# Performance work log

Hardware: AMD Instinct MI355X
Metric: run time of the kernel (lower is better)

## Reference

```python
import jax, jax.numpy as jnp
import numpy as np
from jax import lax

D = 1024      # input_dim
H = 4096      # hidden_dim (4*D)
E = 8         # num_experts
TOPK = 2      # sparse_top_k


def setup_inputs() -> dict:
    key = jax.random.key(0)
    ks = jax.random.split(key, 7)
    s = 0.02
    return {
        "x": jax.random.normal(ks[0], (2, 2048, D), dtype=jnp.float32),
        "W1": jax.random.normal(ks[1], (E, D, H), dtype=jnp.float32) * s,
        "b1": jnp.zeros((E, H), dtype=jnp.float32),
        "W2": jax.random.normal(ks[2], (E, H, D), dtype=jnp.float32) * s,
        "b2": jnp.zeros((E, D), dtype=jnp.float32),
        "Wr": jax.random.normal(ks[3], (D, E), dtype=jnp.float32) * s,
        "br": jnp.zeros((E,), dtype=jnp.float32),
    }


def reference(x, W1, b1, W2, b2, Wr, br):
    B, S, _ = x.shape
    xf = x.reshape(-1, D)                                  # [T, D]
    logits = xf @ Wr + br                                  # [T, E]
    # top-k threshold masking (keep logits >= k-th largest, else -inf)
    topv, _ = lax.top_k(logits, TOPK)                      # [T, k]
    thresh = topv[:, TOPK - 1:TOPK]                        # [T, 1]
    masked = jnp.where(logits >= thresh, logits, -jnp.inf)
    weights = jax.nn.softmax(masked, axis=-1)              # [T, E]
    # run ALL experts densely (faithful to reference), then weighted sum
    h = jax.nn.gelu(jnp.einsum('td,edh->eth', xf, W1) + b1[:, None, :],
                    approximate=False)                     # [E, T, H]
    expert_out = jnp.einsum('eth,ehd->etd', h, W2) + b2[:, None, :]  # [E, T, D]
    out = jnp.einsum('etd,te->td', expert_out, weights)    # [T, D]
    return out.reshape(B, S, D)
```

## Files before the change

kernel.cpp:

```cpp
#include <hip/hip_runtime.h>
#include <math.h>

typedef __bf16 bf16x8 __attribute__((ext_vector_type(8)));
typedef float f32x4 __attribute__((ext_vector_type(4)));

#define DDIM 1024
#define HDIM 4096
#define NE 8
#define TT 4096
#define CAP 9216

static const size_t OFF_CTRL   = 0;
static const size_t OFF_ROWMAP = 256;
static const size_t OFF_WROW   = OFF_ROWMAP + (size_t)CAP * 4;
static const size_t OFF_ROWPOS = OFF_WROW + (size_t)CAP * 4;
static const size_t OFF_TOKE   = OFF_ROWPOS + (size_t)TT * 2 * 4;
static const size_t OFF_TOKW   = OFF_TOKE + (size_t)TT * 2 * 4;
static const size_t OFF_XB     = OFF_TOKW + (size_t)TT * 2 * 4;
static const size_t OFF_W1T    = OFF_XB + (size_t)TT * DDIM * 2;
static const size_t OFF_W2T    = OFF_W1T + (size_t)NE * HDIM * DDIM * 2;
static const size_t OFF_H      = OFF_W2T + (size_t)NE * DDIM * HDIM * 2;
static const size_t OFF_PO     = OFF_H + (size_t)CAP * HDIM * 2;
static const size_t WS_NEED    = OFF_PO + (size_t)CAP * DDIM * 2;

__device__ __forceinline__ unsigned short f2bf(float f) {
  unsigned int u = __builtin_bit_cast(unsigned int, f);
  u = (u + 0x7FFFu + ((u >> 16) & 1u)) >> 16;
  return (unsigned short)u;
}

__device__ __forceinline__ float bf2f(unsigned short s) {
  return __builtin_bit_cast(float, (unsigned int)s << 16);
}

__device__ __forceinline__ void async16(void* lds, const void* g) {
  __builtin_amdgcn_global_load_lds(
      (__attribute__((address_space(1))) void*)g,
      (__attribute__((address_space(3))) void*)lds, 16, 0, 0);
}

__device__ __forceinline__ float gelu_exact(float v) {
  return 0.5f * v * (1.0f + erff(v * 0.70710678118654752f));
}

__global__ __launch_bounds__(256) void router_k(
    const float* __restrict__ x, const float* __restrict__ Wr, const float* __restrict__ br,
    unsigned short* __restrict__ xb, int* __restrict__ toke, float* __restrict__ tokw) {
  int tid = threadIdx.x, lane = tid & 63, wid = tid >> 6;
  int t = blockIdx.x * 4 + wid;
  const float* xr = x + (size_t)t * DDIM;
  float acc[NE];
#pragma unroll
  for (int e = 0; e < NE; ++e) acc[e] = 0.f;
#pragma unroll
  for (int it = 0; it < DDIM / 256; ++it) {
    int d0 = it * 256 + lane * 4;
    float4 xv = *(const float4*)(xr + d0);
    ushort4 xs;
    xs.x = f2bf(xv.x); xs.y = f2bf(xv.y); xs.z = f2bf(xv.z); xs.w = f2bf(xv.w);
    *(ushort4*)(xb + (size_t)t * DDIM + d0) = xs;
    const float4* w0 = (const float4*)(Wr + (size_t)(d0 + 0) * NE);
    const float4* w1 = (const float4*)(Wr + (size_t)(d0 + 1) * NE);
    const float4* w2 = (const float4*)(Wr + (size_t)(d0 + 2) * NE);
    const float4* w3 = (const float4*)(Wr + (size_t)(d0 + 3) * NE);
    float4 a, b;
    a = w0[0]; b = w0[1];
    acc[0] += xv.x * a.x; acc[1] += xv.x * a.y; acc[2] += xv.x * a.z; acc[3] += xv.x * a.w;
    acc[4] += xv.x * b.x; acc[5] += xv.x * b.y; acc[6] += xv.x * b.z; acc[7] += xv.x * b.w;
    a = w1[0]; b = w1[1];
    acc[0] += xv.y * a.x; acc[1] += xv.y * a.y; acc[2] += xv.y * a.z; acc[3] += xv.y * a.w;
    acc[4] += xv.y * b.x; acc[5] += xv.y * b.y; acc[6] += xv.y * b.z; acc[7] += xv.y * b.w;
    a = w2[0]; b = w2[1];
    acc[0] += xv.z * a.x; acc[1] += xv.z * a.y; acc[2] += xv.z * a.z; acc[3] += xv.z * a.w;
    acc[4] += xv.z * b.x; acc[5] += xv.z * b.y; acc[6] += xv.z * b.z; acc[7] += xv.z * b.w;
    a = w3[0]; b = w3[1];
    acc[0] += xv.w * a.x; acc[1] += xv.w * a.y; acc[2] += xv.w * a.z; acc[3] += xv.w * a.w;
    acc[4] += xv.w * b.x; acc[5] += xv.w * b.y; acc[6] += xv.w * b.z; acc[7] += xv.w * b.w;
  }
#pragma unroll
  for (int e = 0; e < NE; ++e) {
#pragma unroll
    for (int s = 32; s > 0; s >>= 1) acc[e] += __shfl_xor(acc[e], s, 64);
  }
  if (lane == 0) {
    float l[NE];
#pragma unroll
    for (int e = 0; e < NE; ++e) l[e] = acc[e] + br[e];
    int i0 = 0; float m0 = l[0];
#pragma unroll
    for (int e = 1; e < NE; ++e) if (l[e] > m0) { m0 = l[e]; i0 = e; }
    int i1 = -1; float m1 = -3.4e38f;
#pragma unroll
    for (int e = 0; e < NE; ++e) if (e != i0 && l[e] > m1) { m1 = l[e]; i1 = e; }
    float e1 = expf(m1 - m0);
    float s = 1.f + e1;
    toke[2 * t] = i0;  toke[2 * t + 1] = i1;
    tokw[2 * t] = 1.f / s;  tokw[2 * t + 1] = e1 / s;
  }
}

__global__ __launch_bounds__(1024) void bin_k(
    const int* __restrict__ toke, const float* __restrict__ tokw,
    int* __restrict__ ctrl, int* __restrict__ rowmap,
    float* __restrict__ wrow, int* __restrict__ rowpos) {
  __shared__ int wcnt[16][8];
  __shared__ int wpre[16][8];
  __shared__ int pbase[9];
  __shared__ int ecnt[8];
  __shared__ int ebase[8];
  int tid = threadIdx.x, lane = tid & 63, w = tid >> 6;

  int myCnt = 0;
  for (int c = 0; c < 8; ++c) {
    int e = toke[c * 1024 + tid];
#pragma unroll
    for (int ee = 0; ee < 8; ++ee) {
      unsigned long long m = __ballot(e == ee);
      if (lane == ee) myCnt += (int)__popcll(m);
    }
  }
  if (lane < 8) wcnt[w][lane] = myCnt;
  __syncthreads();
  if (tid == 0) {
    int off = 0;
    for (int e = 0; e < 8; ++e) {
      int s = 0;
      for (int ww = 0; ww < 16; ++ww) s += wcnt[ww][e];
      ecnt[e] = s;
      pbase[e] = off;
      ebase[e] = off;
      ctrl[8 + e] = off;
      off += ((s + 127) >> 7) << 7;
    }
    pbase[8] = off;
    ctrl[16] = off;
  }
  __syncthreads();

  for (int e = 0; e < 8; ++e) {
    int start = pbase[e] + ecnt[e], end = pbase[e + 1];
    for (int r = start + tid; r < end; r += 1024) { rowmap[r] = 0; wrow[r] = 0.f; }
  }

  for (int c = 0; c < 8; ++c) {
    int slot = c * 1024 + tid;
    int e = toke[slot];
    unsigned long long mown = 0;
#pragma unroll
    for (int ee = 0; ee < 8; ++ee) {
      unsigned long long m = __ballot(e == ee);
      if (lane == ee) wcnt[w][ee] = (int)__popcll(m);
      if (e == ee) mown = m;
    }
    __syncthreads();
    if (tid < 128) {
      int ww = tid >> 3, ee = tid & 7;
      int s = 0;
      for (int p = 0; p < ww; ++p) s += wcnt[p][ee];
      wpre[ww][ee] = s;
    }
    __syncthreads();
    int rank = (int)__popcll(mown & ((1ull << lane) - 1ull));
    int r = ebase[e] + wpre[w][e] + rank;
    rowmap[r] = slot >> 1;
    wrow[r] = tokw[slot];
    rowpos[slot] = r;
    __syncthreads();
    if (tid < 8) {
      int s = 0;
      for (int ww = 0; ww < 16; ++ww) s += wcnt[ww][tid];
      ebase[tid] += s;
    }
    __syncthreads();
  }
}

__global__ __launch_bounds__(256) void convT_k(
    const float* __restrict__ src, unsigned short* __restrict__ dst, int K_, int N_) {
  __shared__ unsigned int lds32[64][33];
  int e = blockIdx.z;
  int kb = blockIdx.y << 6, nb = blockIdx.x << 6;
  int t = threadIdx.x;
  const float* s = src + (size_t)e * K_ * N_ + (size_t)kb * N_ + nb;
  int n0 = (t & 15) << 2;
#pragma unroll
  for (int i = 0; i < 2; ++i) {
    int k2 = (i << 4) + (t >> 4);
    float4 a = *(const float4*)(s + (size_t)(2 * k2) * N_ + n0);
    float4 b = *(const float4*)(s + (size_t)(2 * k2 + 1) * N_ + n0);
    lds32[n0 + 0][k2] = (unsigned)f2bf(a.x) | ((unsigned)f2bf(b.x) << 16);
    lds32[n0 + 1][k2] = (unsigned)f2bf(a.y) | ((unsigned)f2bf(b.y) << 16);
    lds32[n0 + 2][k2] = (unsigned)f2bf(a.z) | ((unsigned)f2bf(b.z) << 16);
    lds32[n0 + 3][k2] = (unsigned)f2bf(a.w) | ((unsigned)f2bf(b.w) << 16);
  }
  __syncthreads();
  unsigned short* dp = dst + (size_t)e * (size_t)N_ * K_ + (size_t)nb * K_ + kb;
  int n = t >> 2, c = t & 3;
  uint4 v0, v1;
  v0.x = lds32[n][(c << 2) + 0]; v0.y = lds32[n][(c << 2) + 1];
  v0.z = lds32[n][(c << 2) + 2]; v0.w = lds32[n][(c << 2) + 3];
  int c4 = (c + 4) << 2;
  v1.x = lds32[n][c4 + 0]; v1.y = lds32[n][c4 + 1];
  v1.z = lds32[n][c4 + 2]; v1.w = lds32[n][c4 + 3];
  *(uint4*)(dp + (size_t)n * K_ + (c << 3)) = v0;
  *(uint4*)(dp + (size_t)n * K_ + ((c + 4) << 3)) = v1;
}

template <int KTOT, int NTOT, bool GATHER, bool DOGELU, bool KSPLIT2>
__global__ __launch_bounds__(256, 2) void gemm_k(
    const unsigned short* __restrict__ A, const unsigned short* __restrict__ Bt,
    const int* __restrict__ ctrl, const int* __restrict__ rowmap,
    const float* __restrict__ wrow, const float* __restrict__ bias,
    unsigned short* __restrict__ out0, unsigned short* __restrict__ out1) {
  __shared__ __align__(16) char SMEM[32768];
  unsigned short* Asm = (unsigned short*)SMEM;
  unsigned short* Bsm = (unsigned short*)(SMEM + 16384);
  int zz = blockIdx.z;
  int e = KSPLIT2 ? (zz & 7) : zz;
  int ks = KSPLIT2 ? (zz >> 3) : 0;
  int off0 = ctrl[8 + e], off1 = ctrl[8 + e + 1];
  int row0 = off0 + (blockIdx.y << 7);
  if (row0 >= off1) return;
  int col0 = blockIdx.x << 7;
  int tid = threadIdx.x, lane = tid & 63, wid = tid >> 6;
  int wr = wid >> 1, wc = wid & 1;
  int kbeg = KSPLIT2 ? ks * (KTOT / 2) : 0;
  int kend = KSPLIT2 ? kbeg + (KTOT / 2) : KTOT;
  unsigned short* outp = (KSPLIT2 && ks) ? out1 : out0;
  if (DOGELU) outp = out0;

  const unsigned short* Asrc[4];
  const unsigned short* Bsrc[4];
#pragma unroll
  for (int c = 0; c < 4; ++c) {
    int ar = row0 + (c << 5) + (tid >> 3);
    size_t arow = GATHER ? (size_t)rowmap[ar] : (size_t)ar;
    Asrc[c] = A + arow * KTOT + ((tid & 7) << 3);
    int brw = col0 + (c << 5) + (tid >> 3);
    Bsrc[c] = Bt + ((size_t)e * NTOT + brw) * KTOT + ((tid & 7) << 3);
  }

  f32x4 acc[4][4];
#pragma unroll
  for (int m = 0; m < 4; ++m)
#pragma unroll
    for (int n = 0; n < 4; ++n) acc[m][n] = (f32x4){0.f, 0.f, 0.f, 0.f};

  int arow_rd = ((wr << 6) + (lane & 15)) << 6;
  int brow_rd = ((wc << 6) + (lane & 15)) << 6;
  int koff = (lane >> 4) << 3;

  for (int k0 = kbeg; k0 < kend; k0 += 64) {
#pragma unroll
    for (int c = 0; c < 4; ++c) {
      async16(SMEM + (((c << 8) + (wid << 6)) << 4), Asrc[c] + k0);
      async16(SMEM + 16384 + (((c << 8) + (wid << 6)) << 4), Bsrc[c] + k0);
    }
    __syncthreads();
#pragma unroll
    for (int kk = 0; kk < 64; kk += 32) {
      bf16x8 af[4], bfr[4];
#pragma unroll
      for (int m = 0; m < 4; ++m)
        af[m] = *(const bf16x8*)&Asm[arow_rd + (m << 10) + kk + koff];
#pragma unroll
      for (int n = 0; n < 4; ++n)
        bfr[n] = *(const bf16x8*)&Bsm[brow_rd + (n << 10) + kk + koff];
#pragma unroll
      for (int m = 0; m < 4; ++m)
#pragma unroll
        for (int n = 0; n < 4; ++n)
          acc[m][n] = __builtin_amdgcn_mfma_f32_16x16x32_bf16(af[m], bfr[n], acc[m][n], 0, 0, 0);
    }
    __syncthreads();
  }

  unsigned short (*Cl)[128] = (unsigned short(*)[128])SMEM;
  int r_b = (lane >> 4) << 2;
  int c_b = lane & 15;
#pragma unroll
  for (int n = 0; n < 4; ++n) {
    int col_l = (wc << 6) + (n << 4) + c_b;
    float bv = (KSPLIT2 && ks) ? 0.f : bias[e * NTOT + col0 + col_l];
#pragma unroll
    for (int m = 0; m < 4; ++m) {
#pragma unroll
      for (int r = 0; r < 4; ++r) {
        int row_l = (wr << 6) + (m << 4) + r_b + r;
        float v = acc[m][n][r] + bv;
        if (DOGELU) {
          Cl[row_l][col_l] = f2bf(gelu_exact(v));
        } else {
          Cl[row_l][col_l] = f2bf(wrow[row0 + row_l] * v);
        }
      }
    }
  }
  __syncthreads();
  int rb = tid >> 4, cof = (tid & 15) << 3;
#pragma unroll
  for (int j = 0; j < 8; ++j) {
    int row_l = rb + (j << 4);
    uint4 v = *(const uint4*)&Cl[row_l][cof];
    *(uint4*)&outp[(size_t)(row0 + row_l) * NTOT + col0 + cof] = v;
  }
}

__global__ __launch_bounds__(256) void gather_k(
    const unsigned short* __restrict__ p0, const unsigned short* __restrict__ p1,
    const int* __restrict__ rowpos, float* __restrict__ out) {
  int t = blockIdx.x, d = threadIdx.x << 2;
  int r0 = rowpos[2 * t], r1 = rowpos[2 * t + 1];
  ushort4 a0 = *(const ushort4*)&p0[(size_t)r0 * DDIM + d];
  ushort4 a1 = *(const ushort4*)&p1[(size_t)r0 * DDIM + d];
  ushort4 b0 = *(const ushort4*)&p0[(size_t)r1 * DDIM + d];
  ushort4 b1 = *(const ushort4*)&p1[(size_t)r1 * DDIM + d];
  float4 o;
  o.x = (bf2f(a0.x) + bf2f(a1.x)) + (bf2f(b0.x) + bf2f(b1.x));
  o.y = (bf2f(a0.y) + bf2f(a1.y)) + (bf2f(b0.y) + bf2f(b1.y));
  o.z = (bf2f(a0.z) + bf2f(a1.z)) + (bf2f(b0.z) + bf2f(b1.z));
  o.w = (bf2f(a0.w) + bf2f(a1.w)) + (bf2f(b0.w) + bf2f(b1.w));
  *(float4*)&out[(size_t)t * DDIM + d] = o;
}

extern "C" void kernel_launch(void* const* d_in, const int* in_sizes, int n_in,
                              void* d_out, int out_size, void* d_ws, size_t ws_size,
                              hipStream_t stream) {
  const float* x  = (const float*)d_in[0];
  const float* W1 = (const float*)d_in[1];
  const float* b1 = (const float*)d_in[2];
  const float* W2 = (const float*)d_in[3];
  const float* b2 = (const float*)d_in[4];
  const float* Wr = (const float*)d_in[5];
  const float* br = (const float*)d_in[6];
  float* out = (float*)d_out;

  if (ws_size < WS_NEED) return;

  char* ws = (char*)d_ws;
  int* ctrl            = (int*)(ws + OFF_CTRL);
  int* rowmap          = (int*)(ws + OFF_ROWMAP);
  float* wrow          = (float*)(ws + OFF_WROW);
  int* rowpos          = (int*)(ws + OFF_ROWPOS);
  int* toke            = (int*)(ws + OFF_TOKE);
  float* tokw          = (float*)(ws + OFF_TOKW);
  unsigned short* xb   = (unsigned short*)(ws + OFF_XB);
  unsigned short* W1T  = (unsigned short*)(ws + OFF_W1T);
  unsigned short* W2T  = (unsigned short*)(ws + OFF_W2T);
  unsigned short* hbuf = (unsigned short*)(ws + OFF_H);
  unsigned short* pout = (unsigned short*)(ws + OFF_PO);
  unsigned short* pout2 = (unsigned short*)(ws + OFF_W1T);

  router_k<<<TT / 4, 256, 0, stream>>>(x, Wr, br, xb, toke, tokw);
  bin_k<<<1, 1024, 0, stream>>>(toke, tokw, ctrl, rowmap, wrow, rowpos);

  convT_k<<<dim3(HDIM / 64, DDIM / 64, NE), 256, 0, stream>>>(W1, W1T, DDIM, HDIM);
  convT_k<<<dim3(DDIM / 64, HDIM / 64, NE), 256, 0, stream>>>(W2, W2T, HDIM, DDIM);

  gemm_k<DDIM, HDIM, true, true, false><<<dim3(HDIM / 128, 32, NE), 256, 0, stream>>>(
      xb, W1T, ctrl, rowmap, wrow, b1, hbuf, nullptr);
  gemm_k<HDIM, DDIM, false, false, true><<<dim3(DDIM / 128, 32, NE * 2), 256, 0, stream>>>(
      hbuf, W2T, ctrl, rowmap, wrow, b2, pout, pout2);

  gather_k<<<TT, 256, 0, stream>>>(pout, pout2, rowpos, out);
}
```

Baseline: 374.6 us.

## Replace first expert GEMM with 256x256-tile, 8-wave, double-buffered pipelined kernel

```diff
diff --git a/kernel.cpp b/kernel.cpp
--- a/kernel.cpp
+++ b/kernel.cpp
@@ -206,36 +206,164 @@
   *(uint4*)(dp + (size_t)n * K_ + ((c + 4) << 3)) = v1;
 }
 
-template <int KTOT, int NTOT, bool GATHER, bool DOGELU, bool KSPLIT2>
-__global__ __launch_bounds__(256, 2) void gemm_k(
+__global__ __launch_bounds__(512, 2) void gemm1_8p(
     const unsigned short* __restrict__ A, const unsigned short* __restrict__ Bt,
     const int* __restrict__ ctrl, const int* __restrict__ rowmap,
-    const float* __restrict__ wrow, const float* __restrict__ bias,
+    const float* __restrict__ bias, unsigned short* __restrict__ outb) {
+  __shared__ __align__(16) char SMEM[131072];
+  int e = blockIdx.z;
+  int off0 = ctrl[8 + e], off1 = ctrl[8 + e + 1];
+  int row0 = off0 + (blockIdx.y << 8);
+  if (row0 >= off1) return;
+  int col0 = blockIdx.x << 8;
+  int tid = threadIdx.x, lane = tid & 63, wid = tid >> 6;
+  int wm = wid >> 2, wn = wid & 3;
+
+  int r_lo = tid >> 2;
+  int ch = (tid & 3) ^ ((r_lo >> 1) & 3);
+  int ar0 = row0 + r_lo;       if (ar0 > off1 - 1) ar0 = off1 - 1;
+  int ar1 = row0 + r_lo + 128; if (ar1 > off1 - 1) ar1 = off1 - 1;
+  const unsigned short* As0 = A + (size_t)rowmap[ar0] * DDIM + (ch << 3);
+  const unsigned short* As1 = A + (size_t)rowmap[ar1] * DDIM + (ch << 3);
+  const unsigned short* Bs0 = Bt + ((size_t)e * HDIM + col0 + r_lo) * DDIM + (ch << 3);
+  const unsigned short* Bs1 = Bt + ((size_t)e * HDIM + col0 + r_lo + 128) * DDIM + (ch << 3);
+  int dstB = tid << 4;
+
+  int rl = lane & 15;
+  int chr = (((lane >> 4) ^ ((rl >> 1) & 3)) << 4);
+  int offA[8], offB[4];
+#pragma unroll
+  for (int m = 0; m < 8; ++m) offA[m] = ((wm << 7) + (m << 4) + rl) * 64 + chr;
+#pragma unroll
+  for (int n = 0; n < 4; ++n) offB[n] = ((wn << 6) + (n << 4) + rl) * 64 + chr;
+
+  f32x4 acc[8][4];
+#pragma unroll
+  for (int m = 0; m < 8; ++m)
+#pragma unroll
+    for (int n = 0; n < 4; ++n) acc[m][n] = (f32x4){0.f, 0.f, 0.f, 0.f};
+  bf16x8 afr[4], bfr[4];
+
+#define SLOT_A(db, kh) ((((db) << 1) | (kh)) * 16384)
+#define SLOT_B(db, kh) (65536 + (((db) << 1) | (kh)) * 16384)
+#define STG_A(db, kh, T) { int go_ = (T) * 64 + (kh) * 32;                    \
+    async16(SMEM + SLOT_A(db, kh) + dstB, As0 + go_);                         \
+    async16(SMEM + SLOT_A(db, kh) + 8192 + dstB, As1 + go_); }
+#define STG_B(db, kh, T) { int go_ = (T) * 64 + (kh) * 32;                    \
+    async16(SMEM + SLOT_B(db, kh) + dstB, Bs0 + go_);                         \
+    async16(SMEM + SLOT_B(db, kh) + 8192 + dstB, Bs1 + go_); }
+#define BAR() asm volatile("s_barrier" ::: "memory")
+#define VMW(N) asm volatile("s_waitcnt vmcnt(" #N ")" ::: "memory")
+#define MFMA16(MB)                                                            \
+  __builtin_amdgcn_s_setprio(1);                                              \
+  _Pragma("unroll") for (int m_ = 0; m_ < 4; ++m_)                            \
+    _Pragma("unroll") for (int n_ = 0; n_ < 4; ++n_)                          \
+      acc[(MB) + m_][n_] = __builtin_amdgcn_mfma_f32_16x16x32_bf16(           \
+          afr[m_], bfr[n_], acc[(MB) + m_][n_], 0, 0, 0);                     \
+  __builtin_amdgcn_s_setprio(0);
+#define PH_A(db, kh, STG)                                                     \
+  { _Pragma("unroll") for (int m_ = 0; m_ < 4; ++m_)                          \
+      afr[m_] = *(const bf16x8*)(SMEM + SLOT_A(db, kh) + offA[m_]);           \
+    _Pragma("unroll") for (int n_ = 0; n_ < 4; ++n_)                          \
+      bfr[n_] = *(const bf16x8*)(SMEM + SLOT_B(db, kh) + offB[n_]);           \
+    STG; BAR(); MFMA16(0); BAR(); }
+#define PH_B(db, kh, STG, VM)                                                 \
+  { _Pragma("unroll") for (int m_ = 0; m_ < 4; ++m_)                          \
+      afr[m_] = *(const bf16x8*)(SMEM + SLOT_A(db, kh) + offA[4 + m_]);       \
+    STG; VM; BAR(); MFMA16(4); BAR(); }
+
+  const int NT = DDIM / 64;
+  STG_A(0, 0, 0); STG_B(0, 0, 0); STG_A(0, 1, 0); STG_B(0, 1, 0);
+  STG_A(1, 0, 1); STG_B(1, 0, 1);
+  VMW(4);
+  BAR();
+
+  for (int U = 0; U + 3 < NT; U += 2) {
+    PH_A(0, 0, STG_A(1, 1, U + 1));
+    PH_B(0, 0, STG_B(1, 1, U + 1), );
+    PH_A(0, 1, STG_A(0, 0, U + 2));
+    PH_B(0, 1, STG_B(0, 0, U + 2), VMW(4));
+    PH_A(1, 0, STG_A(0, 1, U + 2));
+    PH_B(1, 0, STG_B(0, 1, U + 2), );
+    PH_A(1, 1, STG_A(1, 0, U + 3));
+    PH_B(1, 1, STG_B(1, 0, U + 3), VMW(4));
+  }
+  PH_A(0, 0, STG_A(1, 1, NT - 1));
+  PH_B(0, 0, STG_B(1, 1, NT - 1), );
+  PH_A(0, 1, );
+  PH_B(0, 1, , VMW(0));
+  PH_A(1, 0, );
+  PH_B(1, 0, , );
+  PH_A(1, 1, );
+  PH_B(1, 1, , );
+
+#undef PH_B
+#undef PH_A
+#undef MFMA16
+#undef VMW
+#undef BAR
+#undef STG_B
+#undef STG_A
+#undef SLOT_B
+#undef SLOT_A
+
+  __syncthreads();
+  unsigned short (*Cl)[256] = (unsigned short(*)[256])SMEM;
+  int r_b = (lane >> 4) << 2;
+#pragma unroll
+  for (int n = 0; n < 4; ++n) {
+    int col_l = (wn << 6) + (n << 4) + rl;
+    float bv = bias[e * HDIM + col0 + col_l];
+#pragma unroll
+    for (int m = 0; m < 8; ++m) {
+#pragma unroll
+      for (int r = 0; r < 4; ++r) {
+        int row_l = (wm << 7) + (m << 4) + r_b + r;
+        Cl[row_l][col_l] = f2bf(gelu_exact(acc[m][n][r] + bv));
+      }
+    }
+  }
+  __syncthreads();
+  int rb2 = tid >> 5;
+  int ce = (tid & 31) << 3;
+#pragma unroll
+  for (int j = 0; j < 16; ++j) {
+    int row_l = rb2 + (j << 4);
+    int grow = row0 + row_l;
+    if (grow < off1) {
+      uint4 v = *(const uint4*)&Cl[row_l][ce];
+      *(uint4*)&outb[(size_t)grow * HDIM + col0 + ce] = v;
+    }
+  }
+}
+
+template <int KTOT, int NTOT>
+__global__ __launch_bounds__(256, 2) void gemm2_k(
+    const unsigned short* __restrict__ A, const unsigned short* __restrict__ Bt,
+    const int* __restrict__ ctrl, const float* __restrict__ wrow,
+    const float* __restrict__ bias,
     unsigned short* __restrict__ out0, unsigned short* __restrict__ out1) {
   __shared__ __align__(16) char SMEM[32768];
   unsigned short* Asm = (unsigned short*)SMEM;
   unsigned short* Bsm = (unsigned short*)(SMEM + 16384);
   int zz = blockIdx.z;
-  int e = KSPLIT2 ? (zz & 7) : zz;
-  int ks = KSPLIT2 ? (zz >> 3) : 0;
+  int e = zz & 7, ks = zz >> 3;
   int off0 = ctrl[8 + e], off1 = ctrl[8 + e + 1];
   int row0 = off0 + (blockIdx.y << 7);
   if (row0 >= off1) return;
   int col0 = blockIdx.x << 7;
   int tid = threadIdx.x, lane = tid & 63, wid = tid >> 6;
   int wr = wid >> 1, wc = wid & 1;
-  int kbeg = KSPLIT2 ? ks * (KTOT / 2) : 0;
-  int kend = KSPLIT2 ? kbeg + (KTOT / 2) : KTOT;
-  unsigned short* outp = (KSPLIT2 && ks) ? out1 : out0;
-  if (DOGELU) outp = out0;
+  int kbeg = ks * (KTOT / 2);
+  int kend = kbeg + (KTOT / 2);
+  unsigned short* outp = ks ? out1 : out0;
 
   const unsigned short* Asrc[4];
   const unsigned short* Bsrc[4];
 #pragma unroll
   for (int c = 0; c < 4; ++c) {
     int ar = row0 + (c << 5) + (tid >> 3);
-    size_t arow = GATHER ? (size_t)rowmap[ar] : (size_t)ar;
-    Asrc[c] = A + arow * KTOT + ((tid & 7) << 3);
+    Asrc[c] = A + (size_t)ar * KTOT + ((tid & 7) << 3);
     int brw = col0 + (c << 5) + (tid >> 3);
     Bsrc[c] = Bt + ((size_t)e * NTOT + brw) * KTOT + ((tid & 7) << 3);
   }
@@ -281,18 +409,13 @@
 #pragma unroll
   for (int n = 0; n < 4; ++n) {
     int col_l = (wc << 6) + (n << 4) + c_b;
-    float bv = (KSPLIT2 && ks) ? 0.f : bias[e * NTOT + col0 + col_l];
+    float bv = ks ? 0.f : bias[e * NTOT + col0 + col_l];
 #pragma unroll
     for (int m = 0; m < 4; ++m) {
 #pragma unroll
       for (int r = 0; r < 4; ++r) {
         int row_l = (wr << 6) + (m << 4) + r_b + r;
-        float v = acc[m][n][r] + bv;
-        if (DOGELU) {
-          Cl[row_l][col_l] = f2bf(gelu_exact(v));
-        } else {
-          Cl[row_l][col_l] = f2bf(wrow[row0 + row_l] * v);
-        }
+        Cl[row_l][col_l] = f2bf(wrow[row0 + row_l] * (acc[m][n][r] + bv));
       }
     }
   }
@@ -357,10 +480,10 @@
   convT_k<<<dim3(HDIM / 64, DDIM / 64, NE), 256, 0, stream>>>(W1, W1T, DDIM, HDIM);
   convT_k<<<dim3(DDIM / 64, HDIM / 64, NE), 256, 0, stream>>>(W2, W2T, HDIM, DDIM);
 
-  gemm_k<DDIM, HDIM, true, true, false><<<dim3(HDIM / 128, 32, NE), 256, 0, stream>>>(
-      xb, W1T, ctrl, rowmap, wrow, b1, hbuf, nullptr);
-  gemm_k<HDIM, DDIM, false, false, true><<<dim3(DDIM / 128, 32, NE * 2), 256, 0, stream>>>(
-      hbuf, W2T, ctrl, rowmap, wrow, b2, pout, pout2);
+  gemm1_8p<<<dim3(HDIM / 256, 16, NE), 512, 0, stream>>>(
+      xb, W1T, ctrl, rowmap, b1, hbuf);
+  gemm2_k<HDIM, DDIM><<<dim3(DDIM / 128, 32, NE * 2), 256, 0, stream>>>(
+      hbuf, W2T, ctrl, wrow, b2, pout, pout2);
 
   gather_k<<<TT, 256, 0, stream>>>(pout, pout2, rowpos, out);
 }
```

Result: slower. 387.1 us (+3.3%).
